# Performance work log

Measured on AMD Instinct MI355X. Metric: run time of the kernel, lower is better.

The kernel has to match this reference:

```python
import jax, jax.numpy as jnp
import numpy as np

D = 256
H_GRID = 256
W_GRID = 256
N_LAYERS = 6


def _build_edges(H, W):
    # Vectorized equivalent of grid_to_graph's 4-neighbor edge construction.
    ii, jj = np.meshgrid(np.arange(H), np.arange(W), indexing='ij')
    srcs, dsts, feats = [], [], []
    for di, dj in [(-1, 0), (1, 0), (0, -1), (0, 1)]:
        ni, nj = ii + di, jj + dj
        m = (ni >= 0) & (ni < H) & (nj >= 0) & (nj < W)
        s = (ii * W + jj)[m]
        d = (ni * W + nj)[m]
        f = np.stack([
            np.full(s.shape, di, np.float32),
            np.full(s.shape, dj, np.float32),
            (ii[m] / H).astype(np.float32),
            (jj[m] / W).astype(np.float32),
        ], axis=-1)
        srcs.append(s); dsts.append(d); feats.append(f)
    edge_index = np.stack([np.concatenate(srcs), np.concatenate(dsts)]).astype(np.int32)
    edge_feats = np.concatenate(feats).astype(np.float32)
    return edge_index, edge_feats


def setup_inputs() -> dict:
    key = jax.random.key(0)
    ks = jax.random.split(key, 16)
    grid = jax.random.randint(ks[0], (H_GRID, W_GRID), 0, 10, dtype=jnp.int32)
    edge_index_np, edge_feats_np = _build_edges(H_GRID, W_GRID)
    edge_index = jnp.asarray(edge_index_np)
    edge_feats = jnp.asarray(edge_feats_np)

    def lin(k, fan_in, fan_out):
        bound = 1.0 / np.sqrt(fan_in)
        k1, k2 = jax.random.split(k)
        W = jax.random.uniform(k1, (fan_in, fan_out), jnp.float32, -bound, bound)
        b = jax.random.uniform(k2, (fan_out,), jnp.float32, -bound, bound)
        return W, b

    node_W, node_b = lin(ks[1], 1, D)

    def stack_lin(k, fan_in, fan_out):
        keys = jax.random.split(k, N_LAYERS)
        Ws, bs = zip(*[lin(kk, fan_in, fan_out) for kk in keys])
        return jnp.stack(Ws), jnp.stack(bs)

    msg_W1, msg_b1 = stack_lin(ks[2], 2 * D + 4, D)
    msg_W2, msg_b2 = stack_lin(ks[3], D, D)
    upd_W1, upd_b1 = stack_lin(ks[4], 2 * D, D)
    upd_W2, upd_b2 = stack_lin(ks[5], D, D)
    out_W, out_b = lin(ks[6], D, 10)

    return {
        'grid': grid, 'edge_index': edge_index, 'edge_feats': edge_feats,
        'node_W': node_W, 'node_b': node_b,
        'msg_W1': msg_W1, 'msg_b1': msg_b1, 'msg_W2': msg_W2, 'msg_b2': msg_b2,
        'upd_W1': upd_W1, 'upd_b1': upd_b1, 'upd_W2': upd_W2, 'upd_b2': upd_b2,
        'out_W': out_W, 'out_b': out_b,
    }


def reference(grid, edge_index, edge_feats, node_W, node_b,
              msg_W1, msg_b1, msg_W2, msg_b2,
              upd_W1, upd_b1, upd_W2, upd_b2,
              out_W, out_b):
    H, W = grid.shape
    N = H * W
    nodes = grid.astype(jnp.float32).reshape(N, 1)         # [N,1]
    h = nodes @ node_W + node_b                              # [N,D]
    src, tgt = edge_index[0], edge_index[1]

    def layer(h, params):
        mW1, mb1, mW2, mb2, uW1, ub1, uW2, ub2 = params
        # gather per-edge source/target features, run message MLP
        msg_in = jnp.concatenate([h[src], h[tgt], edge_feats], axis=-1)  # [E,2D+4]
        m = jax.nn.relu(msg_in @ mW1 + mb1) @ mW2 + mb2                   # [E,D]
        # scatter-add messages onto target nodes (vectorized segment sum)
        agg = jax.ops.segment_sum(m, tgt, num_segments=N)                 # [N,D]
        u_in = jnp.concatenate([h, agg], axis=-1)                         # [N,2D]
        h_new = jax.nn.relu(u_in @ uW1 + ub1) @ uW2 + ub2                 # [N,D]
        return h_new, None

    h, _ = jax.lax.scan(layer, h, (msg_W1, msg_b1, msg_W2, msg_b2,
                                   upd_W1, upd_b1, upd_W2, upd_b2))
    out = h @ out_W + out_b                                  # [N,10]
    return out.reshape(H, W, 10)
```

## Files before the change

kernel.cpp:

```cpp
#include <hip/hip_runtime.h>

#define HG 256
#define WGD 256
#define NN (HG*WGD)
#define NL 6

typedef _Float16 f16;
typedef _Float16 f16x8 __attribute__((ext_vector_type(8)));
typedef float f32x4 __attribute__((ext_vector_type(4)));

__device__ __forceinline__ void gload_lds16(const f16* g, f16* lds) {
  __builtin_amdgcn_global_load_lds(
      (const __attribute__((address_space(1))) unsigned int*)g,
      (__attribute__((address_space(3))) unsigned int*)lds, 16, 0, 0);
}

template<int KK, int EPI, int DOPQ>
__global__ __launch_bounds__(512,4) void gemm_merge(
    const f16* __restrict__ A, int lda,
    const f16* __restrict__ BtU_,
    const f16* __restrict__ BtPQ_,
    f16* __restrict__ Uo,
    f16* __restrict__ PQo,
    const float* __restrict__ bias,
    const float* __restrict__ v2,
    const float* __restrict__ avec,
    const int* __restrict__ gridv,
    const float* __restrict__ bias2)
{
  constexpr int NT = KK/64;
  __shared__ f16 sh[40960];
  const int tid  = threadIdx.x;
  const int lane = tid & 63;
  const int w    = tid >> 6;

  int bid = blockIdx.x;
  bid = (bid & 7) * 128 + (bid >> 3);
  const int mbase = bid * 64;

  f32x4 acc[4][2];
#pragma unroll
  for (int a=0;a<4;a++)
#pragma unroll
    for (int b=0;b<2;b++) acc[a][b] = (f32x4){0.f,0.f,0.f,0.f};

  const int r8  = lane >> 3;
  const int c8s = ((lane & 7) ^ r8) * 8;

#define ASB(b) (sh + (b)*4096)
#define BSB(b) (sh + 8192 + (b)*16384)
#define UL (sh)
#define BC (sh + 16384)

#define STAGEM(kt, buf)                                                        \
  {                                                                            \
    gload_lds16(A + (size_t)(mbase + w*8 + r8)*lda + (kt)*64 + c8s,            \
                ASB(buf) + w*512);                                             \
    const f16* Bb = BtU_ + (kt)*64;                                            \
    _Pragma("unroll")                                                          \
    for (int p=0;p<4;p++) {                                                    \
      int qc = p*8 + w;                                                        \
      gload_lds16(Bb + (size_t)(qc*8 + r8)*512 + c8s, BSB(buf) + qc*512);      \
    }                                                                          \
  }

  STAGEM(0, 0);
  __syncthreads();
  int cur = 0;
  for (int kt = 0; kt < NT; ++kt) {
    if (kt + 1 < NT) STAGEM(kt + 1, cur ^ 1);
    const f16* Acur = ASB(cur);
    const f16* Bcur = BSB(cur);
#pragma unroll
    for (int ks=0; ks<2; ++ks) {
      const int off = (((ks*4 + (lane>>4)) ^ (lane & 7)) * 8);
      f16x8 af[4], bf[2];
#pragma unroll
      for (int fm=0; fm<4; ++fm)
        af[fm] = *(const f16x8*)&Acur[(fm*16 + (lane&15))*64 + off];
#pragma unroll
      for (int fn=0; fn<2; ++fn)
        bf[fn] = *(const f16x8*)&Bcur[(w*32 + fn*16 + (lane&15))*64 + off];
#pragma unroll
      for (int fm=0; fm<4; ++fm)
#pragma unroll
        for (int fn=0; fn<2; ++fn)
          acc[fm][fn] = __builtin_amdgcn_mfma_f32_16x16x32_f16(af[fm], bf[fn], acc[fm][fn], 0,0,0);
    }
    __syncthreads();
    cur ^= 1;
  }
#undef STAGEM

#pragma unroll
  for (int fm=0; fm<4; ++fm) {
#pragma unroll
    for (int fn=0; fn<2; ++fn) {
      const int coll = w*32 + fn*16 + (lane&15);
#pragma unroll
      for (int r=0;r<4;r++) {
        int rl  = fm*16 + (lane>>4)*4 + r;
        int row = mbase + rl;
        float v = acc[fm][fn][r];
        int i = row >> 8, j = row & 255;
        float deg = (float)((i>0)+(i<255)+(j>0)+(j<255));
        v += bias[coll] + deg * v2[coll];
        if (EPI==3) v += (float)gridv[row] * avec[coll];
        v = fmaxf(v, 0.f);
        f16 hv = (f16)v;
        Uo[(size_t)row*512 + coll] = hv;
        if (DOPQ) {
          int sblk = (coll >> 3) ^ (rl & 7);
          UL[rl*256 + sblk*8 + (coll & 7)] = hv;
        }
      }
    }
  }

  if (DOPQ) {
    __syncthreads();
    for (int h=0; h<2; ++h) {
      f32x4 acc2[4][2];
#pragma unroll
      for (int a=0;a<4;a++)
#pragma unroll
        for (int b=0;b<2;b++) acc2[a][b] = (f32x4){0.f,0.f,0.f,0.f};
      for (int kt=0; kt<4; ++kt) {
        const f16* Bb = BtPQ_ + (size_t)(h*256)*256 + kt*64;
#pragma unroll
        for (int p=0;p<4;p++) {
          int qc = p*8 + w;
          gload_lds16(Bb + (size_t)(qc*8 + r8)*256 + c8s, BC + qc*512);
        }
        __syncthreads();
#pragma unroll
        for (int ks=0; ks<2; ++ks) {
          f16x8 af[4], bf[2];
#pragma unroll
          for (int fm=0; fm<4; ++fm) {
            int rl = fm*16 + (lane&15);
            int sblk = (kt*8 + ks*4 + (lane>>4)) ^ (rl & 7);
            af[fm] = *(const f16x8*)&UL[rl*256 + sblk*8];
          }
#pragma unroll
          for (int fn=0; fn<2; ++fn) {
            int rb = w*32 + fn*16 + (lane&15);
            int offb = (((ks*4 + (lane>>4)) ^ (rb & 7)) * 8);
            bf[fn] = *(const f16x8*)&BC[rb*64 + offb];
          }
#pragma unroll
          for (int fm=0; fm<4; ++fm)
#pragma unroll
            for (int fn=0; fn<2; ++fn)
              acc2[fm][fn] = __builtin_amdgcn_mfma_f32_16x16x32_f16(af[fm], bf[fn], acc2[fm][fn], 0,0,0);
        }
        __syncthreads();
      }
      const float* b2 = bias2 + h*256;
#pragma unroll
      for (int fm=0; fm<4; ++fm) {
#pragma unroll
        for (int fn=0; fn<2; ++fn) {
          const int coll = w*32 + fn*16 + (lane&15);
#pragma unroll
          for (int r=0;r<4;r++) {
            int row = mbase + fm*16 + (lane>>4)*4 + r;
            PQo[(size_t)row*512 + h*256 + coll] = (f16)(acc2[fm][fn][r] + b2[coll]);
          }
        }
      }
    }
  }
#undef ASB
#undef BSB
#undef UL
#undef BC
}

__device__ __forceinline__ void gemm_core256(
    const f16* __restrict__ A, int lda,
    const f16* __restrict__ Bt, int ldb,
    f16* __restrict__ C, int ldc,
    int mbase, int nbase, f16* As, f16* Bs)
{
  const int tid  = threadIdx.x;
  const int lane = tid & 63;
  const int w    = tid >> 6;
  const int wm   = w >> 1, wn = w & 1;

  f32x4 acc[4][4];
#pragma unroll
  for (int a=0;a<4;a++)
#pragma unroll
    for (int b=0;b<4;b++) acc[a][b] = (f32x4){0.f,0.f,0.f,0.f};

  const int r8  = lane >> 3;
  const int c8s = ((lane & 7) ^ r8) * 8;

  for (int kt = 0; kt < 4; ++kt) {
    const f16* Ab = A  + (size_t)(mbase + w*32)*lda + kt*64;
    const f16* Bb = Bt + (size_t)(nbase + w*32)*ldb + kt*64;
#pragma unroll
    for (int i=0;i<4;i++) {
      gload_lds16(Ab + (size_t)(i*8 + r8)*lda + c8s, &As[(w*32+i*8)*64]);
      gload_lds16(Bb + (size_t)(i*8 + r8)*ldb + c8s, &Bs[(w*32+i*8)*64]);
    }
    __syncthreads();
#pragma unroll
    for (int ks=0; ks<2; ++ks) {
      const int off = (((ks*4 + (lane>>4)) ^ (lane & 7)) * 8);
      f16x8 af[4], bf[4];
#pragma unroll
      for (int fm=0; fm<4; ++fm)
        af[fm] = *(const f16x8*)&As[(wm*64 + fm*16 + (lane&15))*64 + off];
#pragma unroll
      for (int fn=0; fn<4; ++fn)
        bf[fn] = *(const f16x8*)&Bs[(wn*64 + fn*16 + (lane&15))*64 + off];
#pragma unroll
      for (int fm=0; fm<4; ++fm)
#pragma unroll
        for (int fn=0; fn<4; ++fn)
          acc[fm][fn] = __builtin_amdgcn_mfma_f32_16x16x32_f16(af[fm], bf[fn], acc[fm][fn], 0,0,0);
    }
    __syncthreads();
  }

  const int row0 = mbase + wm*64 + (lane>>4)*4;
  const int col0 = nbase + wn*64 + (lane&15);
#pragma unroll
  for (int fm=0; fm<4; ++fm)
#pragma unroll
    for (int fn=0; fn<4; ++fn)
#pragma unroll
      for (int r=0;r<4;r++)
        C[(size_t)(row0 + fm*16 + r)*ldc + (col0 + fn*16)] = (f16)acc[fm][fn][r];
}

__global__ __launch_bounds__(256) void fold_all(
    const f16* __restrict__ BtA,  const f16* __restrict__ uW2h,
    const f16* __restrict__ mW2h, const f16* __restrict__ uW1aT,
    const f16* __restrict__ uW1bT,const f16* __restrict__ oWTh,
    f16* __restrict__ BtPQ, f16* __restrict__ BtU, f16* __restrict__ Wp2t)
{
  __shared__ f16 As[128*64];
  __shared__ f16 Bs[128*64];
  const int b = blockIdx.x;
  if (b < 40) {
    int z = b >> 3, rem = b & 7, x = rem & 3, y = rem >> 2;
    gemm_core256(BtA + (size_t)(z+1)*131072, 256, uW2h + (size_t)z*65536, 256,
                 BtPQ + (size_t)(z+1)*131072, 256, x*128, y*128, As, Bs);
  } else if (b < 60) {
    int rem = b - 40, z = rem >> 2, r2 = rem & 3, x = r2 & 1, y = r2 >> 1;
    gemm_core256(uW1aT + (size_t)(z+1)*65536, 256, uW2h + (size_t)z*65536, 256,
                 BtU + (size_t)(z+1)*131072, 512, x*128, y*128, As, Bs);
  } else if (b < 84) {
    int rem = b - 60, z = rem >> 2, r2 = rem & 3, x = r2 & 1, y = r2 >> 1;
    gemm_core256(uW1bT + (size_t)z*65536, 256, mW2h + (size_t)z*65536, 256,
                 BtU + (size_t)z*131072 + 256, 512, x*128, y*128, As, Bs);
  } else {
    int y = b - 84;
    gemm_core256(oWTh, 256, uW2h + (size_t)5*65536, 256,
                 Wp2t, 256, 0, y*128, As, Bs);
  }
}

template<int R1>
__global__ __launch_bounds__(256) void edge_fuse(
    const f16* __restrict__ PQ, f16* __restrict__ UR,
    const float* __restrict__ cvec, const float* __restrict__ wsi_,
    const float* __restrict__ wsj_,
    const int* __restrict__ gridv, const float* __restrict__ pa,
    const float* __restrict__ pc)
{
  const int t  = threadIdx.x;
  const int ln = t >> 5, ch = t & 31;
  int bid = blockIdx.x;
  bid = (bid & 7) * 1024 + (bid >> 3);
  const int n  = bid*8 + ln;
  const int i  = n >> 8, j = n & 255;
  const int co = ch*8;

  float q[8], pa0[8], pc0[8];
  if (R1) {
    float g = (float)gridv[n];
#pragma unroll
    for (int e=0;e<8;e++) {
      pa0[e] = pa[co+e]; pc0[e] = pc[co+e];
      q[e] = g*pa[256+co+e] + pc[256+co+e];
    }
  } else {
    f16x8 qv = *(const f16x8*)&PQ[(size_t)n*512 + 256 + co];
#pragma unroll
    for (int e=0;e<8;e++) q[e] = (float)qv[e];
  }
  float wi[8], wj[8];
#pragma unroll
  for (int e=0;e<8;e++){ wi[e]=wsi_[co+e]; wj[e]=wsj_[co+e]; }
  float acc[8];
#pragma unroll
  for (int e=0;e<8;e++) acc[e]=0.f;

  const int DI[4] = {-1,1,0,0};
  const int DJ[4] = {0,0,-1,1};
#pragma unroll
  for (int d=0; d<4; ++d) {
    int si = i - DI[d], sj = j - DJ[d];
    if (si>=0 && si<HG && sj>=0 && sj<WGD) {
      int s = si*WGD + sj;
      float fsi = si * (1.f/HG), fsj = sj * (1.f/WGD);
      float pvf[8];
      if (R1) {
        float gs = (float)gridv[s];
#pragma unroll
        for (int e=0;e<8;e++) pvf[e] = gs*pa0[e] + pc0[e];
      } else {
        f16x8 pv = *(const f16x8*)&PQ[(size_t)s*512 + co];
#pragma unroll
        for (int e=0;e<8;e++) pvf[e] = (float)pv[e];
      }
#pragma unroll
      for (int e=0;e<8;e++) {
        float v = pvf[e] + q[e] + cvec[d*256+co+e] + fsi*wi[e] + fsj*wj[e];
        acc[e] += fmaxf(v, 0.f);
      }
    }
  }
  f16x8 outv;
#pragma unroll
  for (int e=0;e<8;e++) outv[e] = (f16)acc[e];
  *(f16x8*)&UR[(size_t)n*512 + 256 + co] = outv;
}

__global__ __launch_bounds__(256) void out_mfma(
    const f16* __restrict__ U,
    const f16* __restrict__ Wp2t,
    const float* __restrict__ ob2,
    float* __restrict__ out)
{
  int lane = threadIdx.x & 63;
  int wv   = threadIdx.x >> 6;
  int nbase = blockIdx.x*64 + wv*16;
  f32x4 acc = (f32x4){0.f,0.f,0.f,0.f};
  int r  = lane & 15;
  int kg = (lane >> 4) * 8;
  const f16* Up = U + (size_t)(nbase + r)*512 + kg;
  const f16* Bp = Wp2t + r*256 + kg;
#pragma unroll
  for (int kt=0; kt<8; ++kt) {
    f16x8 af = *(const f16x8*)(Up + kt*32);
    f16x8 bf = *(const f16x8*)(Bp + kt*32);
    acc = __builtin_amdgcn_mfma_f32_16x16x32_f16(af, bf, acc, 0,0,0);
  }
  int col = lane & 15;
  int row0 = (lane>>4)*4;
  if (col < 10) {
    float bo = ob2[col];
#pragma unroll
    for (int rr=0; rr<4; ++rr)
      out[(size_t)(nbase + row0 + rr)*10 + col] = acc[rr] + bo;
  }
}

__global__ __launch_bounds__(256) void prep_small(
    const float* __restrict__ uW2, const float* __restrict__ mW2,
    const float* __restrict__ oW,  const float* __restrict__ mW1,
    const float* __restrict__ mb1, const float* __restrict__ mb2,
    const float* __restrict__ uW1, const float* __restrict__ ub1,
    const float* __restrict__ ub2, const float* __restrict__ nb,
    const float* __restrict__ nW,  const float* __restrict__ ob,
    f16* __restrict__ uW2h, f16* __restrict__ mW2h, f16* __restrict__ oWTh,
    float* __restrict__ cvec, float* __restrict__ wsi_, float* __restrict__ wsj_,
    float* __restrict__ v2, float* __restrict__ ubias, float* __restrict__ avec,
    float* __restrict__ pqb, float* __restrict__ pa, float* __restrict__ pc,
    float* __restrict__ ob2,
    f16* __restrict__ BtA, f16* __restrict__ uW1aT, f16* __restrict__ uW1bT)
{
  __shared__ float red[3][4][64];
  __shared__ float tbuf[32][33];
  const int b = blockIdx.x;
  const int tid = threadIdx.x;
  if (b < 1536) {
    int idx = b*256 + tid;
    uW2h[idx] = (f16)uW2[idx];
    mW2h[idx] = (f16)mW2[idx];
  } else if (b < 1664) {
    int c = b - 1536, j = tid;
    oWTh[c*256 + j] = (c < 10) ? (f16)oW[j*10 + c] : (f16)0.f;
  } else if (b < 1670) {
    int l = b - 1664, j = tid;
    const float* base = mW1 + (size_t)l*516*256;
    float w512 = base[512*256 + j], w513 = base[513*256 + j];
    float b1 = mb1[l*256 + j];
    const int DI[4] = {-1,1,0,0};
    const int DJ[4] = {0,0,-1,1};
    for (int d=0;d<4;d++)
      cvec[(l*4+d)*256 + j] = (float)DI[d]*w512 + (float)DJ[d]*w513 + b1;
    wsi_[l*256+j] = base[514*256 + j];
    wsj_[l*256+j] = base[515*256 + j];
  } else if (b < 1694) {
    int pr = tid & 63, q = tid >> 6;
    int pair = (b-1670)*64 + pr;
    int l = pair >> 8, j = pair & 255;
    const float* prevb = l ? (ub2 + (l-1)*256) : nb;
    float s1=0.f, s2=0.f, s3=0.f;
    for (int t = q*64; t < q*64+64; ++t) {
      s1 += mb2[l*256+t] * uW1[((size_t)l*512+256+t)*256 + j];
      s2 += prevb[t]     * uW1[((size_t)l*512+t)*256 + j];
      if (l==0) s3 += nW[t] * uW1[(size_t)t*256 + j];
    }
    red[0][q][pr]=s1; red[1][q][pr]=s2; red[2][q][pr]=s3;
    __syncthreads();
    if (q==0) {
      float a = red[0][0][pr]+red[0][1][pr]+red[0][2][pr]+red[0][3][pr];
      float bb = red[1][0][pr]+red[1][1][pr]+red[1][2][pr]+red[1][3][pr];
      v2[pair] = a;
      ubias[pair] = ub1[pair] + bb;
      if (l==0) avec[j] = red[2][0][pr]+red[2][1][pr]+red[2][2][pr]+red[2][3][pr];
    }
  } else if (b < 1742) {
    int pr = tid & 63, q = tid >> 6;
    int pair = (b-1694)*64 + pr;
    int l = pair >> 9, c = pair & 511;
    int rowoff = (c < 256) ? 0 : 256;
    int cc = c & 255;
    const float* base = mW1 + (size_t)l*516*256 + (size_t)rowoff*256 + cc;
    float s1=0.f, s2=0.f;
    if (l==0) {
      for (int j=q*64; j<q*64+64; ++j) { float wv = base[(size_t)j*256]; s1 += nW[j]*wv; s2 += nb[j]*wv; }
    } else {
      const float* pb = ub2 + (l-1)*256;
      for (int j=q*64; j<q*64+64; ++j) s1 += pb[j]*base[(size_t)j*256];
    }
    red[0][q][pr]=s1; red[1][q][pr]=s2;
    __syncthreads();
    if (q==0) {
      float a = red[0][0][pr]+red[0][1][pr]+red[0][2][pr]+red[0][3][pr];
      if (l==0) { pa[c]=a; pc[c]=red[1][0][pr]+red[1][1][pr]+red[1][2][pr]+red[1][3][pr]; }
      else pqb[pair] = a;
    }
  } else if (b == 1742) {
    int c = tid >> 4, jg = tid & 15;
    float s = 0.f;
    if (c < 10)
      for (int j=jg*16; j<jg*16+16; ++j) s += ub2[5*256+j]*oW[j*10+c];
    red[0][c>>2][(c&3)*16+jg] = s;
    __syncthreads();
    if (jg==0 && c < 16) {
      float a=0.f;
      for (int t2=0;t2<16;t2++) a += red[0][c>>2][(c&3)*16+t2];
      ob2[c] = (c < 10) ? a + ob[c] : 0.f;
    }
  } else {
    int t = b - 1743;
    int z = t >> 6, rem = t & 63;
    int bxs = (rem & 7) * 32, bys = (rem >> 3) * 32;
    const int q = z / 6, l = z % 6;
    const float* s;
    f16* d;
    if (q == 0)      { s = mW1 + (size_t)l*516*256;          d = BtA   + (size_t)l*131072; }
    else if (q == 1) { s = mW1 + (size_t)l*516*256 + 65536;  d = BtA   + (size_t)l*131072 + 65536; }
    else if (q == 2) { s = uW1 + (size_t)l*131072;           d = uW1aT + (size_t)l*65536; }
    else             { s = uW1 + (size_t)l*131072 + 65536;   d = uW1bT + (size_t)l*65536; }
    const int tx = tid & 31, ty = tid >> 5;
#pragma unroll
    for (int rr=0; rr<4; ++rr)
      tbuf[ty+rr*8][tx] = s[(size_t)(bys+ty+rr*8)*256 + bxs+tx];
    __syncthreads();
#pragma unroll
    for (int rr=0; rr<4; ++rr)
      d[(size_t)(bxs+ty+rr*8)*256 + bys+tx] = (f16)tbuf[tx][ty+rr*8];
  }
}

extern "C" void kernel_launch(void* const* d_in, const int* in_sizes, int n_in,
                              void* d_out, int out_size, void* d_ws, size_t ws_size,
                              hipStream_t stream)
{
  const int*   gridv = (const int*) d_in[0];
  const float* nW   = (const float*)d_in[3];
  const float* nb   = (const float*)d_in[4];
  const float* mW1  = (const float*)d_in[5];
  const float* mb1  = (const float*)d_in[6];
  const float* mW2  = (const float*)d_in[7];
  const float* mb2  = (const float*)d_in[8];
  const float* uW1  = (const float*)d_in[9];
  const float* ub1  = (const float*)d_in[10];
  const float* uW2  = (const float*)d_in[11];
  const float* ub2  = (const float*)d_in[12];
  const float* oW   = (const float*)d_in[13];
  const float* ob   = (const float*)d_in[14];
  float* out = (float*)d_out;

  char* ws = (char*)d_ws;
  size_t off = 0;
  f16* URa  = (f16*)(ws + off); off += (size_t)NN*512*2;
  f16* URb  = (f16*)(ws + off); off += (size_t)NN*512*2;
  f16* PQ   = (f16*)(ws + off); off += (size_t)NN*512*2;
  f16* BtA  = (f16*)(ws + off); off += 6*512*256*2;
  f16* BtPQ = (f16*)(ws + off); off += 6*512*256*2;
  f16* BtU  = (f16*)(ws + off); off += 6*256*512*2;
  f16* uW2h = (f16*)(ws + off); off += 6*256*256*2;
  f16* mW2h = (f16*)(ws + off); off += 6*256*256*2;
  f16* uW1aT= (f16*)(ws + off); off += 6*256*256*2;
  f16* uW1bT= (f16*)(ws + off); off += 6*256*256*2;
  f16* oWTh = (f16*)(ws + off); off += 128*256*2;
  f16* Wp2t = (f16*)(ws + off); off += 128*256*2;
  float* cvec = (float*)(ws + off); off += 6*4*256*4;
  float* wsi_ = (float*)(ws + off); off += 6*256*4;
  float* wsj_ = (float*)(ws + off); off += 6*256*4;
  float* v2   = (float*)(ws + off); off += 6*256*4;
  float* ubias= (float*)(ws + off); off += 6*256*4;
  float* pqb  = (float*)(ws + off); off += 6*512*4;
  float* pa   = (float*)(ws + off); off += 512*4;
  float* pc   = (float*)(ws + off); off += 512*4;
  float* avec = (float*)(ws + off); off += 256*4;
  float* ob2  = (float*)(ws + off); off += 16*4;

  prep_small<<<3279,256,0,stream>>>(uW2, mW2, oW, mW1, mb1, mb2, uW1, ub1, ub2,
                                    nb, nW, ob,
                                    uW2h, mW2h, oWTh, cvec, wsi_, wsj_,
                                    v2, ubias, avec, pqb, pa, pc, ob2,
                                    BtA, uW1aT, uW1bT);
  fold_all<<<86,256,0,stream>>>(BtA, uW2h, mW2h, uW1aT, uW1bT, oWTh,
                                BtPQ, BtU, Wp2t);

  edge_fuse<1><<<8192,256,0,stream>>>(nullptr, URa, cvec, wsi_, wsj_, gridv, pa, pc);
  gemm_merge<256,3,1><<<1024,512,0,stream>>>(
      URa + 256, 512, BtU + 256, BtPQ + (size_t)1*131072,
      URb, PQ, ubias, v2, avec, gridv, pqb + 1*512);

  f16* cur = URb; f16* nxt = URa;
  for (int l=1;l<5;l++){
    edge_fuse<0><<<8192,256,0,stream>>>(PQ, cur, cvec + l*1024, wsi_ + l*256, wsj_ + l*256,
                                        nullptr, nullptr, nullptr);
    gemm_merge<512,1,1><<<1024,512,0,stream>>>(
        cur, 512, BtU + (size_t)l*131072, BtPQ + (size_t)(l+1)*131072,
        nxt, PQ, ubias + l*256, v2 + l*256, nullptr, nullptr, pqb + (l+1)*512);
    f16* t = cur; cur = nxt; nxt = t;
  }

  edge_fuse<0><<<8192,256,0,stream>>>(PQ, cur, cvec + 5*1024, wsi_ + 5*256, wsj_ + 5*256,
                                      nullptr, nullptr, nullptr);
  gemm_merge<512,1,0><<<1024,512,0,stream>>>(
      cur, 512, BtU + (size_t)5*131072, nullptr,
      nxt, nullptr, ubias + 5*256, v2 + 5*256, nullptr, nullptr, nullptr);

  out_mfma<<<1024,256,0,stream>>>(nxt, Wp2t, ob2, out);
}
```

Before: 449.9 us.

## Load B weight fragments directly from global memory instead of staging in LDS

The merged GEMM kernel no longer stages the weight (B) tiles through shared memory. Each wave now reads its B fragments straight from global memory, relying on cache hits because every block shares the same weights. This cuts LDS use from about 80KB to 32KB, so the launch bound is raised to 6 blocks per CU to gain occupancy, and the barriers in the PQ loop are removed. The cost is more global/L2 traffic with uncoalesced 16-byte-per-lane loads whose latency sits directly ahead of the MFMAs, and more register pressure under the tighter launch bound.

New measurement: 784.6 us. +74.4%, slower.

```diff
diff --git a/kernel.cpp b/kernel.cpp
--- a/kernel.cpp
+++ b/kernel.cpp
@@ -16,7 +16,7 @@
 }
 
 template<int KK, int EPI, int DOPQ>
-__global__ __launch_bounds__(512,4) void gemm_merge(
+__global__ __launch_bounds__(512,6) void gemm_merge(
     const f16* __restrict__ A, int lda,
     const f16* __restrict__ BtU_,
     const f16* __restrict__ BtPQ_,
@@ -29,7 +29,7 @@
     const float* __restrict__ bias2)
 {
   constexpr int NT = KK/64;
-  __shared__ f16 sh[40960];
+  __shared__ f16 sh[16384];
   const int tid  = threadIdx.x;
   const int lane = tid & 63;
   const int w    = tid >> 6;
@@ -48,29 +48,18 @@
   const int c8s = ((lane & 7) ^ r8) * 8;
 
 #define ASB(b) (sh + (b)*4096)
-#define BSB(b) (sh + 8192 + (b)*16384)
 #define UL (sh)
-#define BC (sh + 16384)
-
-#define STAGEM(kt, buf)                                                        \
-  {                                                                            \
-    gload_lds16(A + (size_t)(mbase + w*8 + r8)*lda + (kt)*64 + c8s,            \
-                ASB(buf) + w*512);                                             \
-    const f16* Bb = BtU_ + (kt)*64;                                            \
-    _Pragma("unroll")                                                          \
-    for (int p=0;p<4;p++) {                                                    \
-      int qc = p*8 + w;                                                        \
-      gload_lds16(Bb + (size_t)(qc*8 + r8)*512 + c8s, BSB(buf) + qc*512);      \
-    }                                                                          \
-  }
-
-  STAGEM(0, 0);
+
+#define STAGEA(kt, buf)                                                        \
+  gload_lds16(A + (size_t)(mbase + w*8 + r8)*lda + (kt)*64 + c8s,              \
+              ASB(buf) + w*512);
+
+  STAGEA(0, 0);
   __syncthreads();
   int cur = 0;
   for (int kt = 0; kt < NT; ++kt) {
-    if (kt + 1 < NT) STAGEM(kt + 1, cur ^ 1);
+    if (kt + 1 < NT) STAGEA(kt + 1, cur ^ 1);
     const f16* Acur = ASB(cur);
-    const f16* Bcur = BSB(cur);
 #pragma unroll
     for (int ks=0; ks<2; ++ks) {
       const int off = (((ks*4 + (lane>>4)) ^ (lane & 7)) * 8);
@@ -80,7 +69,9 @@
         af[fm] = *(const f16x8*)&Acur[(fm*16 + (lane&15))*64 + off];
 #pragma unroll
       for (int fn=0; fn<2; ++fn)
-        bf[fn] = *(const f16x8*)&Bcur[(w*32 + fn*16 + (lane&15))*64 + off];
+        bf[fn] = *(const f16x8*)(BtU_ +
+                   (size_t)(w*32 + fn*16 + (lane&15))*512 +
+                   kt*64 + ks*32 + (lane>>4)*8);
 #pragma unroll
       for (int fm=0; fm<4; ++fm)
 #pragma unroll
@@ -90,7 +81,7 @@
     __syncthreads();
     cur ^= 1;
   }
-#undef STAGEM
+#undef STAGEA
 
 #pragma unroll
   for (int fm=0; fm<4; ++fm) {
@@ -125,14 +116,8 @@
       for (int a=0;a<4;a++)
 #pragma unroll
         for (int b=0;b<2;b++) acc2[a][b] = (f32x4){0.f,0.f,0.f,0.f};
+#pragma unroll
       for (int kt=0; kt<4; ++kt) {
-        const f16* Bb = BtPQ_ + (size_t)(h*256)*256 + kt*64;
-#pragma unroll
-        for (int p=0;p<4;p++) {
-          int qc = p*8 + w;
-          gload_lds16(Bb + (size_t)(qc*8 + r8)*256 + c8s, BC + qc*512);
-        }
-        __syncthreads();
 #pragma unroll
         for (int ks=0; ks<2; ++ks) {
           f16x8 af[4], bf[2];
@@ -143,18 +128,16 @@
             af[fm] = *(const f16x8*)&UL[rl*256 + sblk*8];
           }
 #pragma unroll
-          for (int fn=0; fn<2; ++fn) {
-            int rb = w*32 + fn*16 + (lane&15);
-            int offb = (((ks*4 + (lane>>4)) ^ (rb & 7)) * 8);
-            bf[fn] = *(const f16x8*)&BC[rb*64 + offb];
-          }
+          for (int fn=0; fn<2; ++fn)
+            bf[fn] = *(const f16x8*)(BtPQ_ +
+                       (size_t)(h*256 + w*32 + fn*16 + (lane&15))*256 +
+                       kt*64 + ks*32 + (lane>>4)*8);
 #pragma unroll
           for (int fm=0; fm<4; ++fm)
 #pragma unroll
             for (int fn=0; fn<2; ++fn)
               acc2[fm][fn] = __builtin_amdgcn_mfma_f32_16x16x32_f16(af[fm], bf[fn], acc2[fm][fn], 0,0,0);
         }
-        __syncthreads();
       }
       const float* b2 = bias2 + h*256;
 #pragma unroll
@@ -172,9 +155,7 @@
     }
   }
 #undef ASB
-#undef BSB
 #undef UL
-#undef BC
 }
 
 __device__ __forceinline__ void gemm_core256(
```
